# Kernel optimization log

Measured on AMD Instinct MI355X. Metric: run time of the kernel, lower is better.

Reference implementation:

```python
import jax, jax.numpy as jnp
import numpy as np

NUM_HEADS = 16
D_MODEL = 1024
DEPTH = D_MODEL // NUM_HEADS


def setup_inputs() -> dict:
    key = jax.random.key(0)
    ks = jax.random.split(key, 9)
    B, S = 2, 2048
    scale = 1.0 / np.sqrt(D_MODEL)
    return {
        "x": jax.random.normal(ks[0], (B, S, D_MODEL), dtype=jnp.float32),
        "wq": jax.random.normal(ks[1], (D_MODEL, D_MODEL), dtype=jnp.float32) * scale,
        "bq": jnp.zeros((D_MODEL,), dtype=jnp.float32),
        "wk": jax.random.normal(ks[2], (D_MODEL, D_MODEL), dtype=jnp.float32) * scale,
        "bk": jnp.zeros((D_MODEL,), dtype=jnp.float32),
        "wv": jax.random.normal(ks[3], (D_MODEL, D_MODEL), dtype=jnp.float32) * scale,
        "bv": jnp.zeros((D_MODEL,), dtype=jnp.float32),
        "wo": jax.random.normal(ks[4], (D_MODEL, D_MODEL), dtype=jnp.float32) * scale,
        "bo": jnp.zeros((D_MODEL,), dtype=jnp.float32),
    }


def _split_heads(t):
    # [B, S, D] -> [B, H, S, depth]
    B, S, _ = t.shape
    return t.reshape(B, S, NUM_HEADS, DEPTH).transpose(0, 2, 1, 3)


def reference(x, wq, bq, wk, bk, wv, bv, wo, bo):
    q = _split_heads(x @ wq + bq)  # [B,H,S,d]
    k = _split_heads(x @ wk + bk)
    v = _split_heads(x @ wv + bv)
    logits = jnp.einsum("bhqd,bhkd->bhqk", q, k) / jnp.sqrt(jnp.float32(DEPTH))
    attn = jax.nn.softmax(logits, axis=-1)  # [B,H,S,S]
    ctx = jnp.einsum("bhqk,bhkd->bhqd", attn, v)
    B, H, S, d = ctx.shape
    concat = ctx.transpose(0, 2, 1, 3).reshape(B, S, D_MODEL)
    out = concat @ wo + bo
    return out, attn
```

## Files before the change

### kernel.cpp

```cpp
#include <hip/hip_runtime.h>
#include <hip/hip_bf16.h>

#define SEQ 2048
#define BATCH 2
#define NH 16
#define DM 1024
#define DEPTH 64
#define MROWS (BATCH * SEQ)

typedef __attribute__((ext_vector_type(8))) short bf16x8;
typedef __attribute__((ext_vector_type(4))) float f32x4;

__device__ __forceinline__ float b2f(ushort u) {
    union { uint i; float f; } v; v.i = ((uint)u) << 16; return v.f;
}
__device__ __forceinline__ ushort f2b(float f) {
    __hip_bfloat16 h = __float2bfloat16(f);
    return *reinterpret_cast<ushort*>(&h);
}

__device__ __forceinline__ void gload_lds16(const void* g, void* l) {
    __builtin_amdgcn_global_load_lds((const __attribute__((address_space(1))) void*)g,
                                     (__attribute__((address_space(3))) void*)l, 16, 0, 0);
}

__global__ __launch_bounds__(256) void convert_f32_bf16(const float* __restrict__ in,
                                                        ushort* __restrict__ outp, int n4) {
    int i = blockIdx.x * 256 + threadIdx.x;
    if (i < n4) {
        const float4 v = ((const float4*)in)[i];
        ushort4 o;
        o.x = f2b(v.x); o.y = f2b(v.y); o.z = f2b(v.z); o.w = f2b(v.w);
        ((ushort4*)outp)[i] = o;
    }
}

__global__ __launch_bounds__(256) void transpose_convert4(const float* __restrict__ w0,
                                                          const float* __restrict__ w1,
                                                          const float* __restrict__ w2,
                                                          const float* __restrict__ w3,
                                                          ushort* __restrict__ WtBase) {
    __shared__ float tile[32][33];
    const int z = blockIdx.z;
    const float* W = (z == 0) ? w0 : (z == 1) ? w1 : (z == 2) ? w2 : w3;
    ushort* Wt = WtBase + (size_t)z * DM * DM;
    const int bx = blockIdx.x * 32;
    const int by = blockIdx.y * 32;
    const int tx = threadIdx.x & 31, ty = threadIdx.x >> 5;
#pragma unroll
    for (int i = 0; i < 32; i += 8)
        tile[ty + i][tx] = W[(size_t)(by + ty + i) * DM + bx + tx];
    __syncthreads();
#pragma unroll
    for (int i = 0; i < 32; i += 8)
        Wt[(size_t)(bx + ty + i) * DM + by + tx] = f2b(tile[tx][ty + i]);
}

__global__ __launch_bounds__(256) void gemm_qkv_mfma(const ushort* __restrict__ A,
                                                     const ushort* __restrict__ WtAll,
                                                     const float* __restrict__ bq,
                                                     const float* __restrict__ bk,
                                                     const float* __restrict__ bv,
                                                     ushort* __restrict__ OutBase) {
    __shared__ __align__(16) ushort As[128 * 32];
    __shared__ __align__(16) ushort Bs[128 * 32];

    const int t    = threadIdx.x;
    const int lane = t & 63;
    const int w    = t >> 6;
    const int wr   = w >> 1, wc = w & 1;
    const int row0 = blockIdx.y * 128;
    const int col0 = blockIdx.x * 128;
    const int bank = col0 >> 10;
    const float* bias = (bank == 0) ? bq : (bank == 1) ? bk : bv;
    const float scale = (bank == 0) ? 0.125f : 1.0f;
    const int ccol0 = col0 & 1023;
    ushort* Cout = OutBase + (size_t)bank * MROWS * DM;

    f32x4 acc[4][4];
#pragma unroll
    for (int mi = 0; mi < 4; ++mi)
#pragma unroll
        for (int ni = 0; ni < 4; ++ni) acc[mi][ni] = (f32x4){0.f, 0.f, 0.f, 0.f};

    const int sr = t >> 2;
    const int sc = (t & 3) * 8;

    for (int k0 = 0; k0 < DM; k0 += 32) {
        gload_lds16(&A[(size_t)(row0 + sr) * DM + k0 + sc],          &As[w * 512]);
        gload_lds16(&A[(size_t)(row0 + 64 + sr) * DM + k0 + sc],     &As[2048 + w * 512]);
        gload_lds16(&WtAll[(size_t)(col0 + sr) * DM + k0 + sc],      &Bs[w * 512]);
        gload_lds16(&WtAll[(size_t)(col0 + 64 + sr) * DM + k0 + sc], &Bs[2048 + w * 512]);
        __syncthreads();

        bf16x8 af[4], bfr[4];
#pragma unroll
        for (int mi = 0; mi < 4; ++mi)
            af[mi] = *(const bf16x8*)&As[(wr * 64 + mi * 16 + (lane & 15)) * 32 + (lane >> 4) * 8];
#pragma unroll
        for (int ni = 0; ni < 4; ++ni)
            bfr[ni] = *(const bf16x8*)&Bs[(wc * 64 + ni * 16 + (lane & 15)) * 32 + (lane >> 4) * 8];
#pragma unroll
        for (int mi = 0; mi < 4; ++mi)
#pragma unroll
            for (int ni = 0; ni < 4; ++ni)
                acc[mi][ni] = __builtin_amdgcn_mfma_f32_16x16x32_bf16(af[mi], bfr[ni], acc[mi][ni], 0, 0, 0);
        __syncthreads();
    }

    float bb[4];
#pragma unroll
    for (int ni = 0; ni < 4; ++ni) bb[ni] = bias[ccol0 + wc * 64 + ni * 16 + (lane & 15)];

#pragma unroll
    for (int mi = 0; mi < 4; ++mi) {
        const int row = row0 + wr * 64 + mi * 16 + (lane >> 4) * 4;
#pragma unroll
        for (int ni = 0; ni < 4; ++ni) {
            const int col = ccol0 + wc * 64 + ni * 16 + (lane & 15);
#pragma unroll
            for (int r = 0; r < 4; ++r)
                Cout[(size_t)(row + r) * DM + col] = f2b((acc[mi][ni][r] + bb[ni]) * scale);
        }
    }
}

__global__ __launch_bounds__(256) void gemm_mfma_f32(const ushort* __restrict__ A,
                                                     const ushort* __restrict__ Wt,
                                                     const float* __restrict__ bias,
                                                     float* __restrict__ Cout) {
    __shared__ __align__(16) ushort As[128 * 32];
    __shared__ __align__(16) ushort Bs[128 * 32];

    const int t    = threadIdx.x;
    const int lane = t & 63;
    const int w    = t >> 6;
    const int wr   = w >> 1, wc = w & 1;
    const int row0 = blockIdx.y * 128;
    const int col0 = blockIdx.x * 128;

    f32x4 acc[4][4];
#pragma unroll
    for (int mi = 0; mi < 4; ++mi)
#pragma unroll
        for (int ni = 0; ni < 4; ++ni) acc[mi][ni] = (f32x4){0.f, 0.f, 0.f, 0.f};

    const int sr = t >> 2;
    const int sc = (t & 3) * 8;

    for (int k0 = 0; k0 < DM; k0 += 32) {
        gload_lds16(&A[(size_t)(row0 + sr) * DM + k0 + sc],       &As[w * 512]);
        gload_lds16(&A[(size_t)(row0 + 64 + sr) * DM + k0 + sc],  &As[2048 + w * 512]);
        gload_lds16(&Wt[(size_t)(col0 + sr) * DM + k0 + sc],      &Bs[w * 512]);
        gload_lds16(&Wt[(size_t)(col0 + 64 + sr) * DM + k0 + sc], &Bs[2048 + w * 512]);
        __syncthreads();

        bf16x8 af[4], bfr[4];
#pragma unroll
        for (int mi = 0; mi < 4; ++mi)
            af[mi] = *(const bf16x8*)&As[(wr * 64 + mi * 16 + (lane & 15)) * 32 + (lane >> 4) * 8];
#pragma unroll
        for (int ni = 0; ni < 4; ++ni)
            bfr[ni] = *(const bf16x8*)&Bs[(wc * 64 + ni * 16 + (lane & 15)) * 32 + (lane >> 4) * 8];
#pragma unroll
        for (int mi = 0; mi < 4; ++mi)
#pragma unroll
            for (int ni = 0; ni < 4; ++ni)
                acc[mi][ni] = __builtin_amdgcn_mfma_f32_16x16x32_bf16(af[mi], bfr[ni], acc[mi][ni], 0, 0, 0);
        __syncthreads();
    }

    float bb[4];
#pragma unroll
    for (int ni = 0; ni < 4; ++ni) bb[ni] = bias[col0 + wc * 64 + ni * 16 + (lane & 15)];

#pragma unroll
    for (int mi = 0; mi < 4; ++mi) {
        const int row = row0 + wr * 64 + mi * 16 + (lane >> 4) * 4;
#pragma unroll
        for (int ni = 0; ni < 4; ++ni) {
            const int col = col0 + wc * 64 + ni * 16 + (lane & 15);
#pragma unroll
            for (int r = 0; r < 4; ++r)
                Cout[(size_t)(row + r) * DM + col] = acc[mi][ni][r] + bb[ni];
        }
    }
}

__global__ __launch_bounds__(256) void transpose_v(const ushort* __restrict__ Vh,
                                                   ushort* __restrict__ Vt3) {
    __shared__ ushort tile[64][80];
    const int t  = threadIdx.x;
    const int bh = blockIdx.x;
    const int cc = blockIdx.y;
    const int k0 = cc * 64;
    const int b  = bh >> 4;
    const int h  = bh & 15;
    const size_t panel = (size_t)b * SEQ * DM + (size_t)h * DEPTH;

    {
        const int k = t >> 2, dc = (t & 3) * 16;
        const ushort* src = Vh + panel + (size_t)(k0 + k) * DM + dc;
        *(bf16x8*)&tile[k][dc]     = *(const bf16x8*)src;
        *(bf16x8*)&tile[k][dc + 8] = *(const bf16x8*)(src + 8);
    }
    __syncthreads();
    {
        const int l  = t & 63;
        const int ni = t >> 6;
        const int kr = (l >> 4) * 8;
        const int dl = ni * 16 + (l & 15);
#pragma unroll
        for (int kh = 0; kh < 2; ++kh) {
            bf16x8 o;
#pragma unroll
            for (int j = 0; j < 8; ++j) o[j] = tile[kh * 32 + kr + j][dl];
            char* dst = (char*)Vt3 +
                        (((size_t)bh * 64 + cc * 2 + kh) * 4 + ni) * 1024 + l * 16;
            *(bf16x8*)dst = o;
        }
    }
}

__global__ __launch_bounds__(512, 2) void attn_fused_kernel(const ushort* __restrict__ Qh,
                                                            const ushort* __restrict__ Kh,
                                                            const ushort* __restrict__ Vt3,
                                                            float* __restrict__ attn_out,
                                                            ushort* __restrict__ Ctx) {
    __shared__ __align__(16) ushort P_lds[16 * 2048];
    __shared__ float red[256];

    const int t    = threadIdx.x;
    const int lane = t & 63;
    const int w    = t >> 6;
    const int qt   = blockIdx.x;
    const int bh   = blockIdx.y;
    const int b    = bh >> 4;
    const int h    = bh & 15;
    const int q0   = qt * 16;
    const int q    = lane & 15;
    const int g    = lane >> 4;
    const int swzP = (q & 7) << 4;

    const size_t panel = (size_t)b * SEQ * DM + (size_t)h * DEPTH;
    char* Pb = (char*)P_lds;

    const ushort* Qrow = Qh + panel + (size_t)(q0 + q) * DM + g * 8;
    const bf16x8 qf0 = *(const bf16x8*)Qrow;
    const bf16x8 qf1 = *(const bf16x8*)(Qrow + 32);

    f32x4 acc[16];
#pragma unroll
    for (int i = 0; i < 16; ++i) acc[i] = (f32x4){0.f, 0.f, 0.f, 0.f};

    const char* Ksrc = (const char*)(Kh + panel);
    const int srow  = t >> 3;
    const int scolb = ((t & 7) * 16) ^ ((srow & 7) << 4);
    char* wavedst = Pb + (t >> 6) * 1024;

#define STAGE_K(c)                                                                  \
    {                                                                               \
        char* dB = wavedst + ((c) & 1) * 32768;                                     \
        _Pragma("unroll")                                                           \
        for (int j = 0; j < 4; ++j) {                                               \
            const char* gp = Ksrc + (size_t)((c) * 256 + j * 64 + srow) * (DM * 2)  \
                             + scolb;                                               \
            gload_lds16(gp, dB + j * 8192);                                         \
        }                                                                           \
    }

    STAGE_K(0);
    __syncthreads();

#pragma unroll
    for (int c = 0; c < 8; ++c) {
        if (c < 7) STAGE_K(c + 1);
        const char* kb = Pb + (c & 1) * 32768;
#pragma unroll
        for (int kt2 = 0; kt2 < 2; ++kt2) {
            const char* rowp = kb + (w * 32 + kt2 * 16 + q) * 128;
            const bf16x8 kf0 = *(const bf16x8*)(rowp + ((g * 16) ^ swzP));
            const bf16x8 kf1 = *(const bf16x8*)(rowp + ((64 + g * 16) ^ swzP));
            acc[c * 2 + kt2] = __builtin_amdgcn_mfma_f32_16x16x32_bf16(kf0, qf0, acc[c * 2 + kt2], 0, 0, 0);
            acc[c * 2 + kt2] = __builtin_amdgcn_mfma_f32_16x16x32_bf16(kf1, qf1, acc[c * 2 + kt2], 0, 0, 0);
        }
        __syncthreads();
    }
#undef STAGE_K

    float mm = acc[0][0];
#pragma unroll
    for (int i = 0; i < 16; ++i) {
#pragma unroll
        for (int r = 0; r < 4; ++r) mm = fmaxf(mm, acc[i][r]);
    }
    mm = fmaxf(mm, __shfl_xor(mm, 16));
    mm = fmaxf(mm, __shfl_xor(mm, 32));
    if (lane < 16) red[w * 16 + lane] = mm;
    __syncthreads();

    float mx = red[q];
#pragma unroll
    for (int ww = 1; ww < 8; ++ww) mx = fmaxf(mx, red[ww * 16 + q]);

    float ssum = 0.f;
#pragma unroll
    for (int i = 0; i < 16; ++i) {
#pragma unroll
        for (int r = 0; r < 4; ++r) {
            const float p = __expf(acc[i][r] - mx);
            acc[i][r] = p;
            ssum += p;
        }
    }
    ssum += __shfl_xor(ssum, 16);
    ssum += __shfl_xor(ssum, 32);
    if (lane < 16) red[128 + w * 16 + lane] = ssum;
    __syncthreads();

    float tot = red[128 + q];
#pragma unroll
    for (int ww = 1; ww < 8; ++ww) tot += red[128 + ww * 16 + q];
    const float rinv = 1.f / tot;

#pragma unroll
    for (int i = 0; i < 16; ++i) {
        const int c2 = i >> 1, kt2 = i & 1;
        const float p0 = acc[i][0] * rinv;
        const float p1 = acc[i][1] * rinv;
        const float p2 = acc[i][2] * rinv;
        const float p3 = acc[i][3] * rinv;
        uint2 uu;
        uu.x = (uint)f2b(p0) | ((uint)f2b(p1) << 16);
        uu.y = (uint)f2b(p2) | ((uint)f2b(p3) << 16);
        *(uint2*)(Pb + q * 4096 + ((c2 * 512 + w * 64 + kt2 * 32 + g * 8) ^ swzP)) = uu;
    }
    __syncthreads();

    float* attn_base = attn_out + ((size_t)bh * SEQ + q0) * SEQ;
#pragma unroll
    for (int it = 0; it < 16; ++it) {
        const int bofs = (w * 512 + lane * 8) ^ ((it & 7) << 4);
        const ushort4 p4 = *(const ushort4*)(Pb + it * 4096 + bofs);
        f32x4 o;
        o[0] = b2f(p4.x); o[1] = b2f(p4.y); o[2] = b2f(p4.z); o[3] = b2f(p4.w);
        __builtin_nontemporal_store(o, (f32x4*)&attn_base[(size_t)it * SEQ + w * 256 + lane * 4]);
    }

    const char* Vf = (const char*)Vt3 + (size_t)bh * 262144;
    f32x4 ctx[4];
#pragma unroll
    for (int ni = 0; ni < 4; ++ni) ctx[ni] = (f32x4){0.f, 0.f, 0.f, 0.f};

#pragma unroll
    for (int c = 0; c < 8; ++c) {
        const bf16x8 af = *(const bf16x8*)(Pb + q * 4096 + ((c * 512 + w * 64 + g * 16) ^ swzP));
        const char* fb = Vf + (size_t)((c * 8 + w) * 4) * 1024 + lane * 16;
#pragma unroll
        for (int ni = 0; ni < 4; ++ni) {
            const bf16x8 bfr = *(const bf16x8*)(fb + ni * 1024);
            ctx[ni] = __builtin_amdgcn_mfma_f32_16x16x32_bf16(af, bfr, ctx[ni], 0, 0, 0);
        }
    }
    __syncthreads();

    float* part = (float*)P_lds;
#pragma unroll
    for (int ni = 0; ni < 4; ++ni) {
#pragma unroll
        for (int r = 0; r < 4; ++r) {
            part[(w * 16 + g * 4 + r) * 64 + ni * 16 + q] = ctx[ni][r];
        }
    }
    __syncthreads();

#pragma unroll
    for (int idx = t; idx < 1024; idx += 512) {
        const int qq = idx >> 6, d = idx & 63;
        float s2 = 0.f;
#pragma unroll
        for (int ww = 0; ww < 8; ++ww) s2 += part[ww * 1024 + idx];
        Ctx[(size_t)(b * SEQ + q0 + qq) * DM + h * DEPTH + d] = f2b(s2);
    }
}

extern "C" void kernel_launch(void* const* d_in, const int* in_sizes, int n_in,
                              void* d_out, int out_size, void* d_ws, size_t ws_size,
                              hipStream_t stream) {
    const float* x  = (const float*)d_in[0];
    const float* wq = (const float*)d_in[1];
    const float* bq = (const float*)d_in[2];
    const float* wk = (const float*)d_in[3];
    const float* bk = (const float*)d_in[4];
    const float* wv = (const float*)d_in[5];
    const float* bv = (const float*)d_in[6];
    const float* wo = (const float*)d_in[7];
    const float* bo = (const float*)d_in[8];

    float* out  = (float*)d_out;
    float* attn = out + (size_t)MROWS * DM;

    ushort* ws  = (ushort*)d_ws;
    ushort* xb  = ws;
    ushort* wqt = xb + (size_t)MROWS * DM;
    ushort* wot = wqt + (size_t)3 * DM * DM;
    ushort* Qh  = wot + (size_t)DM * DM;
    ushort* Kh  = Qh + (size_t)MROWS * DM;
    ushort* Vh  = Kh + (size_t)MROWS * DM;
    ushort* cxb = Vh + (size_t)MROWS * DM;
    ushort* Vt3 = cxb + (size_t)MROWS * DM;

    convert_f32_bf16<<<dim3(MROWS * DM / 4 / 256), 256, 0, stream>>>(x, xb, MROWS * DM / 4);
    transpose_convert4<<<dim3(DM / 32, DM / 32, 4), 256, 0, stream>>>(wq, wk, wv, wo, wqt);

    gemm_qkv_mfma<<<dim3(3 * DM / 128, MROWS / 128), 256, 0, stream>>>(xb, wqt, bq, bk, bv, Qh);

    transpose_v<<<dim3(BATCH * NH, SEQ / 64), 256, 0, stream>>>(Vh, Vt3);

    attn_fused_kernel<<<dim3(SEQ / 16, BATCH * NH), 512, 0, stream>>>(Qh, Kh, Vt3, attn, cxb);

    gemm_mfma_f32<<<dim3(DM / 128, MROWS / 128), 256, 0, stream>>>(cxb, wot, bo, out);
}
```

Measured before the change: 222.6 us.

## Pre-pack K into MFMA fragment layout and load it directly from global

```diff
diff --git a/kernel.cpp b/kernel.cpp
--- a/kernel.cpp
+++ b/kernel.cpp
@@ -222,8 +222,43 @@
     }
 }
 
+__global__ __launch_bounds__(256) void transpose_k(const ushort* __restrict__ Kh,
+                                                   ushort* __restrict__ Kf) {
+    __shared__ ushort tile[64][80];
+    const int t  = threadIdx.x;
+    const int bh = blockIdx.x;
+    const int cc = blockIdx.y;
+    const int k0 = cc * 64;
+    const int b  = bh >> 4;
+    const int h  = bh & 15;
+    const size_t panel = (size_t)b * SEQ * DM + (size_t)h * DEPTH;
+
+    {
+        const int k = t >> 2, dc = (t & 3) * 16;
+        const ushort* src = Kh + panel + (size_t)(k0 + k) * DM + dc;
+        *(bf16x8*)&tile[k][dc]     = *(const bf16x8*)src;
+        *(bf16x8*)&tile[k][dc + 8] = *(const bf16x8*)(src + 8);
+    }
+    __syncthreads();
+    {
+        const int l   = t & 63;
+        const int sub = t >> 6;
+        const int row = sub * 16 + (l & 15);
+        const int db  = (l >> 4) * 8;
+#pragma unroll
+        for (int ks = 0; ks < 2; ++ks) {
+            bf16x8 o;
+#pragma unroll
+            for (int j = 0; j < 8; ++j) o[j] = tile[row][ks * 32 + db + j];
+            char* dst = (char*)Kf +
+                        ((((size_t)bh * 128 + cc * 4 + sub) * 2) + ks) * 1024 + l * 16;
+            *(bf16x8*)dst = o;
+        }
+    }
+}
+
 __global__ __launch_bounds__(512, 2) void attn_fused_kernel(const ushort* __restrict__ Qh,
-                                                            const ushort* __restrict__ Kh,
+                                                            const ushort* __restrict__ Kfrag,
                                                             const ushort* __restrict__ Vt3,
                                                             float* __restrict__ attn_out,
                                                             ushort* __restrict__ Ctx) {
@@ -249,44 +284,19 @@
     const bf16x8 qf0 = *(const bf16x8*)Qrow;
     const bf16x8 qf1 = *(const bf16x8*)(Qrow + 32);
 
+    const char* Kf = (const char*)Kfrag + (size_t)bh * 262144;
     f32x4 acc[16];
 #pragma unroll
     for (int i = 0; i < 16; ++i) acc[i] = (f32x4){0.f, 0.f, 0.f, 0.f};
 
-    const char* Ksrc = (const char*)(Kh + panel);
-    const int srow  = t >> 3;
-    const int scolb = ((t & 7) * 16) ^ ((srow & 7) << 4);
-    char* wavedst = Pb + (t >> 6) * 1024;
-
-#define STAGE_K(c)                                                                  \
-    {                                                                               \
-        char* dB = wavedst + ((c) & 1) * 32768;                                     \
-        _Pragma("unroll")                                                           \
-        for (int j = 0; j < 4; ++j) {                                               \
-            const char* gp = Ksrc + (size_t)((c) * 256 + j * 64 + srow) * (DM * 2)  \
-                             + scolb;                                               \
-            gload_lds16(gp, dB + j * 8192);                                         \
-        }                                                                           \
-    }
-
-    STAGE_K(0);
-    __syncthreads();
-
-#pragma unroll
-    for (int c = 0; c < 8; ++c) {
-        if (c < 7) STAGE_K(c + 1);
-        const char* kb = Pb + (c & 1) * 32768;
-#pragma unroll
-        for (int kt2 = 0; kt2 < 2; ++kt2) {
-            const char* rowp = kb + (w * 32 + kt2 * 16 + q) * 128;
-            const bf16x8 kf0 = *(const bf16x8*)(rowp + ((g * 16) ^ swzP));
-            const bf16x8 kf1 = *(const bf16x8*)(rowp + ((64 + g * 16) ^ swzP));
-            acc[c * 2 + kt2] = __builtin_amdgcn_mfma_f32_16x16x32_bf16(kf0, qf0, acc[c * 2 + kt2], 0, 0, 0);
-            acc[c * 2 + kt2] = __builtin_amdgcn_mfma_f32_16x16x32_bf16(kf1, qf1, acc[c * 2 + kt2], 0, 0, 0);
-        }
-        __syncthreads();
-    }
-#undef STAGE_K
+#pragma unroll
+    for (int i = 0; i < 16; ++i) {
+        const char* fb = Kf + (size_t)((w * 16 + i) * 2) * 1024 + lane * 16;
+        const bf16x8 kf0 = *(const bf16x8*)fb;
+        const bf16x8 kf1 = *(const bf16x8*)(fb + 1024);
+        acc[i] = __builtin_amdgcn_mfma_f32_16x16x32_bf16(kf0, qf0, acc[i], 0, 0, 0);
+        acc[i] = __builtin_amdgcn_mfma_f32_16x16x32_bf16(kf1, qf1, acc[i], 0, 0, 0);
+    }
 
     float mm = acc[0][0];
 #pragma unroll
@@ -325,7 +335,6 @@
 
 #pragma unroll
     for (int i = 0; i < 16; ++i) {
-        const int c2 = i >> 1, kt2 = i & 1;
         const float p0 = acc[i][0] * rinv;
         const float p1 = acc[i][1] * rinv;
         const float p2 = acc[i][2] * rinv;
@@ -333,7 +342,7 @@
         uint2 uu;
         uu.x = (uint)f2b(p0) | ((uint)f2b(p1) << 16);
         uu.y = (uint)f2b(p2) | ((uint)f2b(p3) << 16);
-        *(uint2*)(Pb + q * 4096 + ((c2 * 512 + w * 64 + kt2 * 32 + g * 8) ^ swzP)) = uu;
+        *(uint2*)(Pb + q * 4096 + ((w * 512 + i * 32 + g * 8) ^ swzP)) = uu;
     }
     __syncthreads();
 
@@ -353,9 +362,9 @@
     for (int ni = 0; ni < 4; ++ni) ctx[ni] = (f32x4){0.f, 0.f, 0.f, 0.f};
 
 #pragma unroll
-    for (int c = 0; c < 8; ++c) {
-        const bf16x8 af = *(const bf16x8*)(Pb + q * 4096 + ((c * 512 + w * 64 + g * 16) ^ swzP));
-        const char* fb = Vf + (size_t)((c * 8 + w) * 4) * 1024 + lane * 16;
+    for (int s8 = 0; s8 < 8; ++s8) {
+        const bf16x8 af = *(const bf16x8*)(Pb + q * 4096 + ((w * 512 + s8 * 64 + g * 16) ^ swzP));
+        const char* fb = Vf + (size_t)((w * 8 + s8) * 4) * 1024 + lane * 16;
 #pragma unroll
         for (int ni = 0; ni < 4; ++ni) {
             const bf16x8 bfr = *(const bf16x8*)(fb + ni * 1024);
@@ -409,6 +418,7 @@
     ushort* Vh  = Kh + (size_t)MROWS * DM;
     ushort* cxb = Vh + (size_t)MROWS * DM;
     ushort* Vt3 = cxb + (size_t)MROWS * DM;
+    ushort* Kf  = Vt3 + (size_t)BATCH * NH * DEPTH * SEQ;
 
     convert_f32_bf16<<<dim3(MROWS * DM / 4 / 256), 256, 0, stream>>>(x, xb, MROWS * DM / 4);
     transpose_convert4<<<dim3(DM / 32, DM / 32, 4), 256, 0, stream>>>(wq, wk, wv, wo, wqt);
@@ -416,8 +426,9 @@
     gemm_qkv_mfma<<<dim3(3 * DM / 128, MROWS / 128), 256, 0, stream>>>(xb, wqt, bq, bk, bv, Qh);
 
     transpose_v<<<dim3(BATCH * NH, SEQ / 64), 256, 0, stream>>>(Vh, Vt3);
-
-    attn_fused_kernel<<<dim3(SEQ / 16, BATCH * NH), 512, 0, stream>>>(Qh, Kh, Vt3, attn, cxb);
+    transpose_k<<<dim3(BATCH * NH, SEQ / 64), 256, 0, stream>>>(Kh, Kf);
+
+    attn_fused_kernel<<<dim3(SEQ / 16, BATCH * NH), 512, 0, stream>>>(Qh, Kf, Vt3, attn, cxb);
 
     gemm_mfma_f32<<<dim3(DM / 128, MROWS / 128), 256, 0, stream>>>(cxb, wot, bo, out);
 }
```

Measured after the change: 219.8 us (median of 2 runs). No clear change (-1.2%).
